# Optimization experiments

Hardware: AMD Instinct MI355X
Metric: run time of the kernel (lower is better)

Reference implementation:

```python
import jax, jax.numpy as jnp
import numpy as np

USER_NUM = 100000
ITEM_NUM = 50000
N_NODES = USER_NUM + ITEM_NUM
EMB_DIM = 64
N_LAYERS = 3
NNZ = 4800000


def setup_inputs() -> dict:
    key = jax.random.key(0)
    k1, k2, k3, k4, k5 = jax.random.split(key, 5)
    user_emb = 0.2 * jax.random.normal(k1, (USER_NUM, EMB_DIM), dtype=jnp.float32)
    item_emb = 0.2 * jax.random.normal(k2, (ITEM_NUM, EMB_DIM), dtype=jnp.float32)
    adj_row = jax.random.randint(k3, (NNZ,), 0, N_NODES, dtype=jnp.int32)
    adj_col = jax.random.randint(k4, (NNZ,), 0, N_NODES, dtype=jnp.int32)
    adj_vals = jax.random.uniform(k5, (NNZ,), dtype=jnp.float32)
    return {
        "user_emb": user_emb,
        "item_emb": item_emb,
        "adj_row": adj_row,
        "adj_col": adj_col,
        "adj_vals": adj_vals,
    }


def _spmm(row, col, vals, x):
    # sparse [N,N] @ dense [N,D] via gather + weighted segment-sum
    msg = vals[:, None] * x[col]  # [nnz, D]
    return jax.ops.segment_sum(msg, row, num_segments=N_NODES)


def reference(user_emb, item_emb, adj_row, adj_col, adj_vals):
    ego = jnp.concatenate([user_emb, item_emb], axis=0)  # [N, D]
    acc = ego  # running sum over layers (equivalent to stack+mean)
    for _ in range(N_LAYERS):
        ego = _spmm(adj_row, adj_col, adj_vals, ego)
        acc = acc + ego
    out = acc / jnp.asarray(N_LAYERS + 1, dtype=acc.dtype)
    return out[:USER_NUM], out[USER_NUM:]
```

## Files before the change

### kernel.cpp

```cpp
#include <hip/hip_runtime.h>

#define USER_NUM 100000
#define ITEM_NUM 50000
#define N_NODES  150000
#define EMB_DIM  64
#define NNZ      4800000

#define CB_SHIFT 10
#define ROWS_PER_CB 1024
#define NCB ((N_NODES + ROWS_PER_CB - 1) / ROWS_PER_CB)
#define CB_CAP 34000
#define TILE 8192
#define NTILES ((NNZ + TILE - 1) / TILE)
#define EPT 32

__device__ __forceinline__ float bflo(unsigned u) {
    return __uint_as_float(u << 16);
}
__device__ __forceinline__ float bfhi(unsigned u) {
    return __uint_as_float(u & 0xFFFF0000u);
}
__device__ __forceinline__ unsigned f2bf(float f) {
    unsigned u = __float_as_uint(f);
    return (u + 0x7FFFu + ((u >> 16) & 1u)) >> 16;
}

__global__ void lgcn_init(const float4* __restrict__ user,
                          const float4* __restrict__ item,
                          uint4* __restrict__ xb) {
    int i = blockIdx.x * blockDim.x + threadIdx.x;
    if (i >= N_NODES * 8) return;
    const int user_chunks = USER_NUM * 8;
    float4 f0, f1;
    if (i < user_chunks) {
        f0 = user[i * 2];
        f1 = user[i * 2 + 1];
    } else {
        f0 = item[(i - user_chunks) * 2];
        f1 = item[(i - user_chunks) * 2 + 1];
    }
    uint4 p;
    p.x = f2bf(f0.x) | (f2bf(f0.y) << 16);
    p.y = f2bf(f0.z) | (f2bf(f0.w) << 16);
    p.z = f2bf(f1.x) | (f2bf(f1.y) << 16);
    p.w = f2bf(f1.z) | (f2bf(f1.w) << 16);
    xb[i] = p;
}

__global__ void lgcn_bcur_init(int* __restrict__ bucket_cursor) {
    int b = blockIdx.x * blockDim.x + threadIdx.x;
    if (b < NCB) bucket_cursor[b] = b * CB_CAP;
}

__global__ __launch_bounds__(256) void lgcn_partition(
    const int* __restrict__ row,
    const int* __restrict__ col,
    const float* __restrict__ vals,
    int* __restrict__ bucket_cursor,
    int2* __restrict__ t_cv) {
    __shared__ int hist[NCB];
    __shared__ int excl[NCB];
    __shared__ int delta[NCB];
    __shared__ unsigned lslot[TILE];
    __shared__ int sscan[256];

    int tid = threadIdx.x;
    int tileStart = blockIdx.x * TILE;
    int tileCount = NNZ - tileStart;
    if (tileCount > TILE) tileCount = TILE;

    for (int b = tid; b < NCB; b += 256) hist[b] = 0;
    __syncthreads();

    int rws[EPT];
#pragma unroll
    for (int k = 0; k < EPT; ++k) {
        int le = tid + k * 256;
        int r = -1;
        if (le < tileCount) {
            r = row[tileStart + le];
            atomicAdd(&hist[r >> CB_SHIFT], 1);
        }
        rws[k] = r;
    }
    __syncthreads();

    int h = (tid < NCB) ? hist[tid] : 0;
    sscan[tid] = h;
    __syncthreads();
    for (int off = 1; off < 256; off <<= 1) {
        int x = (tid >= off) ? sscan[tid - off] : 0;
        __syncthreads();
        sscan[tid] += x;
        __syncthreads();
    }
    if (tid < NCB) {
        int ex = sscan[tid] - h;
        excl[tid] = ex;
        int rb = h ? atomicAdd(&bucket_cursor[tid], h) : 0;
        delta[tid] = rb - ex;
    }
    __syncthreads();

#pragma unroll
    for (int k = 0; k < EPT; ++k) {
        int le = tid + k * 256;
        if (le < tileCount) {
            int r = rws[k];
            int b = r >> CB_SHIFT;
            int lp = atomicAdd(&excl[b], 1);
            lslot[lp] = ((unsigned)b << 23) |
                        ((unsigned)(r & (ROWS_PER_CB - 1)) << 13) |
                        (unsigned)le;
        }
    }
    __syncthreads();

    for (int i = tid; i < tileCount; i += 256) {
        unsigned s = lslot[i];
        int b = s >> 23;
        int rlo = (s >> 13) & (ROWS_PER_CB - 1);
        int le = s & 8191;
        int e = tileStart + le;
        int gpos = delta[b] + i;
        if (gpos < (b + 1) * CB_CAP) {
            t_cv[gpos] = make_int2((rlo << 18) | col[e],
                                   __float_as_int(vals[e]));
        }
    }
}

__global__ __launch_bounds__(1024) void lgcn_finalize(
    const int* __restrict__ bucket_cursor,
    const int2* __restrict__ t_cv,
    int2* __restrict__ csr_cv,
    int2* __restrict__ row_se) {
    __shared__ int hist[ROWS_PER_CB];
    __shared__ int cur[ROWS_PER_CB];
    __shared__ int sscan[1024];
    int t = threadIdx.x;
    int b = blockIdx.x;

    int v = 0;
    if (t < NCB) {
        int cb = bucket_cursor[t] - t * CB_CAP;
        v = (cb > CB_CAP) ? CB_CAP : cb;
    }
    if (t < 256) sscan[t] = v;
    __syncthreads();
    for (int off = 1; off < 256; off <<= 1) {
        int x = 0;
        if (t < 256 && t >= off) x = sscan[t - off];
        __syncthreads();
        if (t < 256) sscan[t] += x;
        __syncthreads();
    }
    int prev = (b == 0) ? 0 : sscan[b - 1];
    int bbase = prev;
    int count = sscan[b] - prev;
    __syncthreads();

    int lo = b * ROWS_PER_CB;
    int nrows = N_NODES - lo;
    if (nrows > ROWS_PER_CB) nrows = ROWS_PER_CB;

    hist[t] = 0;
    __syncthreads();

    int base = b * CB_CAP;
    int eEnd = base + count;
    int e = base + t;
    for (; e + 3 * 1024 < eEnd; e += 4 * 1024) {
        int2 c0 = t_cv[e];
        int2 c1 = t_cv[e + 1024];
        int2 c2 = t_cv[e + 2048];
        int2 c3 = t_cv[e + 3072];
        atomicAdd(&hist[(unsigned)c0.x >> 18], 1);
        atomicAdd(&hist[(unsigned)c1.x >> 18], 1);
        atomicAdd(&hist[(unsigned)c2.x >> 18], 1);
        atomicAdd(&hist[(unsigned)c3.x >> 18], 1);
    }
    for (; e < eEnd; e += 1024)
        atomicAdd(&hist[(unsigned)t_cv[e].x >> 18], 1);
    __syncthreads();

    int h = hist[t];
    sscan[t] = h;
    __syncthreads();
    for (int off = 1; off < 1024; off <<= 1) {
        int x = (t >= off) ? sscan[t - off] : 0;
        __syncthreads();
        sscan[t] += x;
        __syncthreads();
    }
    int p = bbase + sscan[t] - h;
    if (t < nrows) {
        row_se[lo + t] = make_int2(p, p + h);
        cur[t] = p;
    }
    __syncthreads();

    e = base + t;
    for (; e + 3 * 1024 < eEnd; e += 4 * 1024) {
        int2 c0 = t_cv[e];
        int2 c1 = t_cv[e + 1024];
        int2 c2 = t_cv[e + 2048];
        int2 c3 = t_cv[e + 3072];
        int p0 = atomicAdd(&cur[(unsigned)c0.x >> 18], 1);
        int p1 = atomicAdd(&cur[(unsigned)c1.x >> 18], 1);
        int p2 = atomicAdd(&cur[(unsigned)c2.x >> 18], 1);
        int p3 = atomicAdd(&cur[(unsigned)c3.x >> 18], 1);
        csr_cv[p0] = make_int2(c0.x & 0x3FFFF, c0.y);
        csr_cv[p1] = make_int2(c1.x & 0x3FFFF, c1.y);
        csr_cv[p2] = make_int2(c2.x & 0x3FFFF, c2.y);
        csr_cv[p3] = make_int2(c3.x & 0x3FFFF, c3.y);
    }
    for (; e < eEnd; e += 1024) {
        int2 cv = t_cv[e];
        int pos = atomicAdd(&cur[(unsigned)cv.x >> 18], 1);
        csr_cv[pos] = make_int2(cv.x & 0x3FFFF, cv.y);
    }
}

#define FMA8(vv, uu) do {                                          \
    a[0] += (vv) * bflo((uu).x); a[1] += (vv) * bfhi((uu).x);      \
    a[2] += (vv) * bflo((uu).y); a[3] += (vv) * bfhi((uu).y);      \
    a[4] += (vv) * bflo((uu).z); a[5] += (vv) * bfhi((uu).z);      \
    a[6] += (vv) * bflo((uu).w); a[7] += (vv) * bfhi((uu).w);      \
} while (0)

#define SPMM_BODY                                                  \
    int gid = blockIdx.x * blockDim.x + threadIdx.x;               \
    int r = gid >> 6;                                              \
    if (r >= N_NODES) return;                                      \
    int lane = threadIdx.x & 63;                                   \
    int c = lane & 7;                                              \
    int sub = lane >> 3;                                           \
    int2 se = row_se[r];                                           \
    int start = se.x;                                              \
    int end = se.y;                                                \
    float a[8] = {0.f, 0.f, 0.f, 0.f, 0.f, 0.f, 0.f, 0.f};         \
    int e = start + sub;                                           \
    for (; e + 24 < end; e += 32) {                                \
        int2 cv0 = csr_cv[e];                                      \
        int2 cv1 = csr_cv[e + 8];                                  \
        int2 cv2 = csr_cv[e + 16];                                 \
        int2 cv3 = csr_cv[e + 24];                                 \
        uint4 u0 = xb[cv0.x * 8 + c];                              \
        uint4 u1 = xb[cv1.x * 8 + c];                              \
        uint4 u2 = xb[cv2.x * 8 + c];                              \
        uint4 u3 = xb[cv3.x * 8 + c];                              \
        float v0 = __int_as_float(cv0.y);                          \
        float v1 = __int_as_float(cv1.y);                          \
        float v2 = __int_as_float(cv2.y);                          \
        float v3 = __int_as_float(cv3.y);                          \
        FMA8(v0, u0);                                              \
        FMA8(v1, u1);                                              \
        FMA8(v2, u2);                                              \
        FMA8(v3, u3);                                              \
    }                                                              \
    if (e + 8 < end) {                                             \
        int2 cv0 = csr_cv[e];                                      \
        int2 cv1 = csr_cv[e + 8];                                  \
        uint4 u0 = xb[cv0.x * 8 + c];                              \
        uint4 u1 = xb[cv1.x * 8 + c];                              \
        float v0 = __int_as_float(cv0.y);                          \
        float v1 = __int_as_float(cv1.y);                          \
        FMA8(v0, u0);                                              \
        FMA8(v1, u1);                                              \
        e += 16;                                                   \
    }                                                              \
    if (e < end) {                                                 \
        int2 cv = csr_cv[e];                                       \
        uint4 u = xb[cv.x * 8 + c];                                \
        float v = __int_as_float(cv.y);                            \
        FMA8(v, u);                                                \
    }                                                              \
    _Pragma("unroll")                                              \
    for (int k = 0; k < 8; ++k) {                                  \
        a[k] += __shfl_xor(a[k], 8);                               \
        a[k] += __shfl_xor(a[k], 16);                              \
        a[k] += __shfl_xor(a[k], 32);                              \
    }

__global__ __launch_bounds__(256, 8) void lgcn_spmm_bf16(
    const int2* __restrict__ row_se,
    const int2* __restrict__ csr_cv,
    const uint4* __restrict__ xb,
    uint4* __restrict__ yb) {
    SPMM_BODY
    if (sub == 0) {
        uint4 p;
        p.x = f2bf(a[0]) | (f2bf(a[1]) << 16);
        p.y = f2bf(a[2]) | (f2bf(a[3]) << 16);
        p.z = f2bf(a[4]) | (f2bf(a[5]) << 16);
        p.w = f2bf(a[6]) | (f2bf(a[7]) << 16);
        yb[r * 8 + c] = p;
    }
}

__global__ __launch_bounds__(256, 8) void lgcn_spmm_final(
    const int2* __restrict__ row_se,
    const int2* __restrict__ csr_cv,
    const uint4* __restrict__ xb,
    const uint4* __restrict__ y1b,
    const float4* __restrict__ user,
    const float4* __restrict__ item,
    float4* __restrict__ out) {
    SPMM_BODY
    if (sub == 0) {
        const float4* src = (r < USER_NUM) ? (user + (size_t)r * 16)
                                           : (item + (size_t)(r - USER_NUM) * 16);
        float4 f0 = src[c * 2];
        float4 f1 = src[c * 2 + 1];
        uint4 q1 = y1b[r * 8 + c];
        uint4 q2 = xb[r * 8 + c];
        float4 o0, o1;
        o0.x = (f0.x + bflo(q1.x) + bflo(q2.x) + a[0]) * 0.25f;
        o0.y = (f0.y + bfhi(q1.x) + bfhi(q2.x) + a[1]) * 0.25f;
        o0.z = (f0.z + bflo(q1.y) + bflo(q2.y) + a[2]) * 0.25f;
        o0.w = (f0.w + bfhi(q1.y) + bfhi(q2.y) + a[3]) * 0.25f;
        o1.x = (f1.x + bflo(q1.z) + bflo(q2.z) + a[4]) * 0.25f;
        o1.y = (f1.y + bfhi(q1.z) + bfhi(q2.z) + a[5]) * 0.25f;
        o1.z = (f1.z + bflo(q1.w) + bflo(q2.w) + a[6]) * 0.25f;
        o1.w = (f1.w + bfhi(q1.w) + bfhi(q2.w) + a[7]) * 0.25f;
        int idx = r * 16 + c * 2;
        out[idx] = o0;
        out[idx + 1] = o1;
    }
}

extern "C" void kernel_launch(void* const* d_in, const int* in_sizes, int n_in,
                              void* d_out, int out_size, void* d_ws, size_t ws_size,
                              hipStream_t stream) {
    const float* user_emb = (const float*)d_in[0];
    const float* item_emb = (const float*)d_in[1];
    const int*   adj_row  = (const int*)d_in[2];
    const int*   adj_col  = (const int*)d_in[3];
    const float* adj_vals = (const float*)d_in[4];
    float* out = (float*)d_out;

    char* base = (char*)d_ws;
    uint4* xb_a   = (uint4*)base;
    int2*  csr_cv = (int2*)(base + 19200000);
    char*  S      = base + 57600000;
    const size_t T_ENTRIES = (size_t)NCB * CB_CAP;
    int2*  t_cv   = (int2*)S;
    uint4* y1b    = (uint4*)S;
    uint4* y2b    = (uint4*)(S + 19200000);
    char*  tail   = S + T_ENTRIES * 8;
    int2*  row_se = (int2*)tail;
    int*   bucket_cursor = (int*)(tail + (size_t)N_NODES * 8);

    {
        int threads = 256;
        int blocks = (N_NODES * 8 + threads - 1) / threads;
        lgcn_init<<<blocks, threads, 0, stream>>>(
            (const float4*)user_emb, (const float4*)item_emb, xb_a);
    }

    lgcn_bcur_init<<<1, 256, 0, stream>>>(bucket_cursor);
    lgcn_partition<<<NTILES, 256, 0, stream>>>(
        adj_row, adj_col, adj_vals, bucket_cursor, t_cv);
    lgcn_finalize<<<NCB, 1024, 0, stream>>>(
        bucket_cursor, t_cv, csr_cv, row_se);

    const int spmm_block = 256;
    const int spmm_grid = (N_NODES * 64 + spmm_block - 1) / spmm_block;
    lgcn_spmm_bf16<<<spmm_grid, spmm_block, 0, stream>>>(
        row_se, csr_cv, xb_a, y1b);
    lgcn_spmm_bf16<<<spmm_grid, spmm_block, 0, stream>>>(
        row_se, csr_cv, y1b, y2b);
    lgcn_spmm_final<<<spmm_grid, spmm_block, 0, stream>>>(
        row_se, csr_cv, y2b, y1b,
        (const float4*)user_emb, (const float4*)item_emb, (float4*)out);
}
```

Measured before the change: 524.7 us.

## Map eight lanes per row and degree-sort rows for balanced SpMM

Each SpMM row is now handled by 8 lanes, one 16-byte chunk each, walking edges sequentially four at a time. Previously 64 lanes split each row eight ways and combined the results with cross-lane shuffles. Three new small kernels build a row permutation sorted by degree, using a histogram, a scan and a placement pass, so rows of similar length share a wavefront. The final layer now reads the layer-0 embedding from the bf16 copy instead of the fp32 inputs. The aim is to remove shuffle reductions and idle lanes, at the cost of longer per-thread dependency chains, extra launches and slightly lower precision for the x0 term.

```diff
diff --git a/kernel.cpp b/kernel.cpp
--- a/kernel.cpp
+++ b/kernel.cpp
@@ -47,9 +47,11 @@
     xb[i] = p;
 }
 
-__global__ void lgcn_bcur_init(int* __restrict__ bucket_cursor) {
+__global__ void lgcn_setup(int* __restrict__ bucket_cursor,
+                           int* __restrict__ deg_hist) {
     int b = blockIdx.x * blockDim.x + threadIdx.x;
     if (b < NCB) bucket_cursor[b] = b * CB_CAP;
+    if (b < 128) deg_hist[b] = 0;
 }
 
 __global__ __launch_bounds__(256) void lgcn_partition(
@@ -222,6 +224,61 @@
     }
 }
 
+__global__ __launch_bounds__(256) void lgcn_deghist(
+    const int2* __restrict__ row_se, int* __restrict__ deg_hist) {
+    __shared__ int lh[128];
+    int t = threadIdx.x;
+    if (t < 128) lh[t] = 0;
+    __syncthreads();
+    int r = blockIdx.x * 256 + t;
+    if (r < N_NODES) {
+        int2 se = row_se[r];
+        int d = se.y - se.x;
+        if (d > 127) d = 127;
+        atomicAdd(&lh[d], 1);
+    }
+    __syncthreads();
+    if (t < 128 && lh[t]) atomicAdd(&deg_hist[t], lh[t]);
+}
+
+__global__ void lgcn_degscan(const int* __restrict__ deg_hist,
+                             int* __restrict__ deg_base) {
+    __shared__ int s[128];
+    int t = threadIdx.x;
+    int v = deg_hist[127 - t];
+    s[t] = v;
+    __syncthreads();
+    for (int off = 1; off < 128; off <<= 1) {
+        int x = (t >= off) ? s[t - off] : 0;
+        __syncthreads();
+        s[t] += x;
+        __syncthreads();
+    }
+    deg_base[127 - t] = s[t] - v;
+}
+
+__global__ __launch_bounds__(256) void lgcn_permplace(
+    const int2* __restrict__ row_se, int* __restrict__ deg_base,
+    int* __restrict__ perm) {
+    __shared__ int lh[128];
+    __shared__ int gb[128];
+    int t = threadIdx.x;
+    if (t < 128) lh[t] = 0;
+    __syncthreads();
+    int r = blockIdx.x * 256 + t;
+    int d = 0, lp = 0;
+    if (r < N_NODES) {
+        int2 se = row_se[r];
+        d = se.y - se.x;
+        if (d > 127) d = 127;
+        lp = atomicAdd(&lh[d], 1);
+    }
+    __syncthreads();
+    if (t < 128 && lh[t]) gb[t] = atomicAdd(&deg_base[t], lh[t]);
+    __syncthreads();
+    if (r < N_NODES) perm[gb[d] + lp] = r;
+}
+
 #define FMA8(vv, uu) do {                                          \
     a[0] += (vv) * bflo((uu).x); a[1] += (vv) * bfhi((uu).x);      \
     a[2] += (vv) * bflo((uu).y); a[3] += (vv) * bfhi((uu).y);      \
@@ -229,23 +286,21 @@
     a[6] += (vv) * bflo((uu).w); a[7] += (vv) * bfhi((uu).w);      \
 } while (0)
 
-#define SPMM_BODY                                                  \
+#define SPMM3_BODY                                                 \
     int gid = blockIdx.x * blockDim.x + threadIdx.x;               \
-    int r = gid >> 6;                                              \
-    if (r >= N_NODES) return;                                      \
-    int lane = threadIdx.x & 63;                                   \
-    int c = lane & 7;                                              \
-    int sub = lane >> 3;                                           \
-    int2 se = row_se[r];                                           \
-    int start = se.x;                                              \
+    int rs = gid >> 3;                                             \
+    if (rs >= N_NODES) return;                                     \
+    int c = threadIdx.x & 7;                                       \
+    int row = perm[rs];                                            \
+    int2 se = row_se[row];                                         \
+    int e = se.x;                                                  \
     int end = se.y;                                                \
     float a[8] = {0.f, 0.f, 0.f, 0.f, 0.f, 0.f, 0.f, 0.f};         \
-    int e = start + sub;                                           \
-    for (; e + 24 < end; e += 32) {                                \
+    for (; e + 3 < end; e += 4) {                                  \
         int2 cv0 = csr_cv[e];                                      \
-        int2 cv1 = csr_cv[e + 8];                                  \
-        int2 cv2 = csr_cv[e + 16];                                 \
-        int2 cv3 = csr_cv[e + 24];                                 \
+        int2 cv1 = csr_cv[e + 1];                                  \
+        int2 cv2 = csr_cv[e + 2];                                  \
+        int2 cv3 = csr_cv[e + 3];                                  \
         uint4 u0 = xb[cv0.x * 8 + c];                              \
         uint4 u1 = xb[cv1.x * 8 + c];                              \
         uint4 u2 = xb[cv2.x * 8 + c];                              \
@@ -259,75 +314,63 @@
         FMA8(v2, u2);                                              \
         FMA8(v3, u3);                                              \
     }                                                              \
-    if (e + 8 < end) {                                             \
+    if (e < end) {     \
+        int last = end - 1;                                        \
+        int e1 = (e + 1 < end) ? e + 1 : last;                     \
+        int e2 = (e + 2 < end) ? e + 2 : last;                     \
         int2 cv0 = csr_cv[e];                                      \
-        int2 cv1 = csr_cv[e + 8];                                  \
+        int2 cv1 = csr_cv[e1];                                     \
+        int2 cv2 = csr_cv[e2];                                     \
         uint4 u0 = xb[cv0.x * 8 + c];                              \
         uint4 u1 = xb[cv1.x * 8 + c];                              \
+        uint4 u2 = xb[cv2.x * 8 + c];                              \
         float v0 = __int_as_float(cv0.y);                          \
-        float v1 = __int_as_float(cv1.y);                          \
+        float v1 = (e + 1 < end) ? __int_as_float(cv1.y) : 0.f;    \
+        float v2 = (e + 2 < end) ? __int_as_float(cv2.y) : 0.f;    \
         FMA8(v0, u0);                                              \
         FMA8(v1, u1);                                              \
-        e += 16;                                                   \
-    }                                                              \
-    if (e < end) {                                                 \
-        int2 cv = csr_cv[e];                                       \
-        uint4 u = xb[cv.x * 8 + c];                                \
-        float v = __int_as_float(cv.y);                            \
-        FMA8(v, u);                                                \
-    }                                                              \
-    _Pragma("unroll")                                              \
-    for (int k = 0; k < 8; ++k) {                                  \
-        a[k] += __shfl_xor(a[k], 8);                               \
-        a[k] += __shfl_xor(a[k], 16);                              \
-        a[k] += __shfl_xor(a[k], 32);                              \
+        FMA8(v2, u2);                                              \
     }
 
 __global__ __launch_bounds__(256, 8) void lgcn_spmm_bf16(
+    const int* __restrict__ perm,
     const int2* __restrict__ row_se,
     const int2* __restrict__ csr_cv,
     const uint4* __restrict__ xb,
     uint4* __restrict__ yb) {
-    SPMM_BODY
-    if (sub == 0) {
-        uint4 p;
-        p.x = f2bf(a[0]) | (f2bf(a[1]) << 16);
-        p.y = f2bf(a[2]) | (f2bf(a[3]) << 16);
-        p.z = f2bf(a[4]) | (f2bf(a[5]) << 16);
-        p.w = f2bf(a[6]) | (f2bf(a[7]) << 16);
-        yb[r * 8 + c] = p;
-    }
+    SPMM3_BODY
+    uint4 p;
+    p.x = f2bf(a[0]) | (f2bf(a[1]) << 16);
+    p.y = f2bf(a[2]) | (f2bf(a[3]) << 16);
+    p.z = f2bf(a[4]) | (f2bf(a[5]) << 16);
+    p.w = f2bf(a[6]) | (f2bf(a[7]) << 16);
+    yb[row * 8 + c] = p;
 }
 
 __global__ __launch_bounds__(256, 8) void lgcn_spmm_final(
+    const int* __restrict__ perm,
     const int2* __restrict__ row_se,
     const int2* __restrict__ csr_cv,
     const uint4* __restrict__ xb,
+    const uint4* __restrict__ x0b,
     const uint4* __restrict__ y1b,
-    const float4* __restrict__ user,
-    const float4* __restrict__ item,
     float4* __restrict__ out) {
-    SPMM_BODY
-    if (sub == 0) {
-        const float4* src = (r < USER_NUM) ? (user + (size_t)r * 16)
-                                           : (item + (size_t)(r - USER_NUM) * 16);
-        float4 f0 = src[c * 2];
-        float4 f1 = src[c * 2 + 1];
-        uint4 q1 = y1b[r * 8 + c];
-        uint4 q2 = xb[r * 8 + c];
-        float4 o0, o1;
-        o0.x = (f0.x + bflo(q1.x) + bflo(q2.x) + a[0]) * 0.25f;
-        o0.y = (f0.y + bfhi(q1.x) + bfhi(q2.x) + a[1]) * 0.25f;
-        o0.z = (f0.z + bflo(q1.y) + bflo(q2.y) + a[2]) * 0.25f;
-        o0.w = (f0.w + bfhi(q1.y) + bfhi(q2.y) + a[3]) * 0.25f;
-        o1.x = (f1.x + bflo(q1.z) + bflo(q2.z) + a[4]) * 0.25f;
-        o1.y = (f1.y + bfhi(q1.z) + bfhi(q2.z) + a[5]) * 0.25f;
-        o1.z = (f1.z + bflo(q1.w) + bflo(q2.w) + a[6]) * 0.25f;
-        o1.w = (f1.w + bfhi(q1.w) + bfhi(q2.w) + a[7]) * 0.25f;
-        int idx = r * 16 + c * 2;
-        out[idx] = o0;
-        out[idx + 1] = o1;
-    }
+    SPMM3_BODY
+    uint4 q0 = x0b[row * 8 + c];
+    uint4 q1 = y1b[row * 8 + c];
+    uint4 q2 = xb[row * 8 + c];
+    float4 o0, o1;
+    o0.x = (bflo(q0.x) + bflo(q1.x) + bflo(q2.x) + a[0]) * 0.25f;
+    o0.y = (bfhi(q0.x) + bfhi(q1.x) + bfhi(q2.x) + a[1]) * 0.25f;
+    o0.z = (bflo(q0.y) + bflo(q1.y) + bflo(q2.y) + a[2]) * 0.25f;
+    o0.w = (bfhi(q0.y) + bfhi(q1.y) + bfhi(q2.y) + a[3]) * 0.25f;
+    o1.x = (bflo(q0.z) + bflo(q1.z) + bflo(q2.z) + a[4]) * 0.25f;
+    o1.y = (bfhi(q0.z) + bfhi(q1.z) + bfhi(q2.z) + a[5]) * 0.25f;
+    o1.z = (bflo(q0.w) + bflo(q1.w) + bflo(q2.w) + a[6]) * 0.25f;
+    o1.w = (bfhi(q0.w) + bfhi(q1.w) + bfhi(q2.w) + a[7]) * 0.25f;
+    int idx = row * 16 + c * 2;
+    out[idx] = o0;
+    out[idx + 1] = o1;
 }
 
 extern "C" void kernel_launch(void* const* d_in, const int* in_sizes, int n_in,
@@ -348,9 +391,12 @@
     int2*  t_cv   = (int2*)S;
     uint4* y1b    = (uint4*)S;
     uint4* y2b    = (uint4*)(S + 19200000);
+    int*   perm   = (int*)(S + 38400000);
     char*  tail   = S + T_ENTRIES * 8;
     int2*  row_se = (int2*)tail;
     int*   bucket_cursor = (int*)(tail + (size_t)N_NODES * 8);
+    int*   deg_hist = bucket_cursor + 256;
+    int*   deg_base = deg_hist + 128;
 
     {
         int threads = 256;
@@ -359,19 +405,23 @@
             (const float4*)user_emb, (const float4*)item_emb, xb_a);
     }
 
-    lgcn_bcur_init<<<1, 256, 0, stream>>>(bucket_cursor);
+    lgcn_setup<<<1, 256, 0, stream>>>(bucket_cursor, deg_hist);
     lgcn_partition<<<NTILES, 256, 0, stream>>>(
         adj_row, adj_col, adj_vals, bucket_cursor, t_cv);
     lgcn_finalize<<<NCB, 1024, 0, stream>>>(
         bucket_cursor, t_cv, csr_cv, row_se);
 
+    const int pblocks = (N_NODES + 255) / 256;
+    lgcn_deghist<<<pblocks, 256, 0, stream>>>(row_se, deg_hist);
+    lgcn_degscan<<<1, 128, 0, stream>>>(deg_hist, deg_base);
+    lgcn_permplace<<<pblocks, 256, 0, stream>>>(row_se, deg_base, perm);
+
     const int spmm_block = 256;
-    const int spmm_grid = (N_NODES * 64 + spmm_block - 1) / spmm_block;
+    const int spmm_grid = (N_NODES * 8 + spmm_block - 1) / spmm_block;
     lgcn_spmm_bf16<<<spmm_grid, spmm_block, 0, stream>>>(
-        row_se, csr_cv, xb_a, y1b);
+        perm, row_se, csr_cv, xb_a, y1b);
     lgcn_spmm_bf16<<<spmm_grid, spmm_block, 0, stream>>>(
-        row_se, csr_cv, y1b, y2b);
+        perm, row_se, csr_cv, y1b, y2b);
     lgcn_spmm_final<<<spmm_grid, spmm_block, 0, stream>>>(
-        row_se, csr_cv, y2b, y1b,
-        (const float4*)user_emb, (const float4*)item_emb, (float4*)out);
-}
+        perm, row_se, csr_cv, y2b, xb_a, y1b, (float4*)out);
+}
```

New measurement: 556.4 us. 6.1% more time.
